# Performance work log

Measured on AMD Instinct MI355X. Metric: run time of the kernel, lower is better.

The kernel has to match this reference:

```python
import jax, jax.numpy as jnp
import numpy as np

DIM = 4096
DEPTH = 13  # complete binary tree, 2**DEPTH - 1 nodes
N_NODES = 2 ** DEPTH - 1


def setup_inputs() -> dict:
    key = jax.random.key(0)
    ks = jax.random.split(key, 9)
    inp = {
        "tree_vec": jax.random.normal(ks[0], (N_NODES, DIM), dtype=jnp.float32),
        "depth": DEPTH,
        # diagonal gate parameters (original shape (dim,1), flattened to (dim,))
        "w_for": jax.random.normal(ks[1], (DIM,), dtype=jnp.float32),
        "u_for": jax.random.normal(ks[2], (DIM,), dtype=jnp.float32),
        "b_for": jnp.zeros((DIM,), dtype=jnp.float32),
        "w_in": jax.random.normal(ks[3], (DIM,), dtype=jnp.float32),
        "u_in": jax.random.normal(ks[4], (DIM,), dtype=jnp.float32),
        "b_in": jnp.zeros((DIM,), dtype=jnp.float32),
        "w_ce": jax.random.normal(ks[5], (DIM,), dtype=jnp.float32),
        "u_ce": jax.random.normal(ks[6], (DIM,), dtype=jnp.float32),
        "b_ce": jnp.zeros((DIM,), dtype=jnp.float32),
        "w_out": jax.random.normal(ks[7], (DIM,), dtype=jnp.float32),
        "u_out": jax.random.normal(ks[8], (DIM,), dtype=jnp.float32),
        "b_out": jnp.zeros((DIM,), dtype=jnp.float32),
    }
    return inp


def _node_gates(x, h_sum, f_sum, p):
    # x, h_sum, f_sum: (n, dim); p: dict of (dim,) params
    it = jax.nn.sigmoid(p["w_in"] * x + p["u_in"] * h_sum + p["b_in"])
    gt = jnp.tanh(p["w_ce"] * x + p["u_ce"] * h_sum + p["b_ce"])
    # NOTE: faithful to the original — forget sum is added raw, not multiplied by child c
    ct = it * gt + f_sum
    ot = jax.nn.sigmoid(p["w_out"] * x + p["u_out"] * h_sum + p["b_out"])
    ht = ot * jnp.tanh(ct)
    return ht, ct


def reference(tree_vec, depth, w_for, u_for, b_for, w_in, u_in, b_in,
              w_ce, u_ce, b_ce, w_out, u_out, b_out):
    p = dict(w_for=w_for, u_for=u_for, b_for=b_for, w_in=w_in, u_in=u_in,
             b_in=b_in, w_ce=w_ce, u_ce=u_ce, b_ce=b_ce, w_out=w_out,
             u_out=u_out, b_out=b_out)
    dim = tree_vec.shape[1]

    # ---- leaf level (original gives leaves one all-zero child row) ----
    L = depth - 1
    n = 2 ** L
    x = tree_vec[2 ** L - 1: 2 ** (L + 1) - 1]          # (n, dim)
    h_sum = jnp.zeros_like(x)                            # sum of zero child h
    f_sum = jax.nn.sigmoid(w_for * x + b_for)            # u_for * 0 dropped
    h, c = _node_gates(x, h_sum, f_sum, p)

    # ---- internal levels, bottom-up ----
    for l in range(depth - 2, -1, -1):
        n = 2 ** l
        x = tree_vec[2 ** l - 1: 2 ** (l + 1) - 1]       # (n, dim)
        h_ch = h.reshape(n, 2, dim)                      # children h
        h_sum = h_ch.sum(axis=1)
        f_sum = jax.nn.sigmoid(w_for * x[:, None, :] + u_for * h_ch + b_for).sum(axis=1)
        h, c = _node_gates(x, h_sum, f_sum, p)

    # root outputs, original shape (dim, 1)
    return h[0].reshape(dim, 1), c[0].reshape(dim, 1)
```

## Files before the change

### kernel.cpp

```cpp
#include <hip/hip_runtime.h>

#define DIM 4096

typedef float v2f __attribute__((ext_vector_type(2)));

constexpr float LOG2E = 1.44269504088896340736f;
constexpr float TWO_LOG2E = 2.0f * LOG2E;

__device__ __forceinline__ float fexp2s(float x) { return __builtin_amdgcn_exp2f(x); }
__device__ __forceinline__ float frcps(float x) { return __builtin_amdgcn_rcpf(x); }

__device__ __forceinline__ v2f expv(v2f u) {
  v2f r; r.x = fexp2s(u.x); r.y = fexp2s(u.y); return r;
}
__device__ __forceinline__ v2f rcpv(v2f u) {
  v2f r; r.x = frcps(u.x); r.y = frcps(u.y); return r;
}
__device__ __forceinline__ v2f fmav(v2f a, v2f b, v2f c) {
  return __builtin_elementwise_fma(a, b, c);
}
__device__ __forceinline__ v2f eclampv(v2f u) {
  v2f c30 = {30.0f, 30.0f};
  return expv(__builtin_elementwise_min(-u, c30));
}

struct P2pk {
  v2f wf, uf, bf;
  v2f wi, ui, bi;
  v2f wc, uc, bc;
  v2f wo, uo, bo;
};

__device__ __forceinline__ v2f ldv(const float* p) { return *(const v2f*)p; }
__device__ __forceinline__ v2f ldscale(const float* p, int d2, float s) {
  return ldv(p + d2) * s;
}

__device__ __forceinline__ P2pk load_params_pk(
    int d2,
    const float* wf, const float* uf, const float* bf,
    const float* wi, const float* ui, const float* bi,
    const float* wc, const float* uc, const float* bc,
    const float* wo, const float* uo, const float* bo) {
  P2pk p;
  p.wf = ldscale(wf, d2, LOG2E);     p.uf = ldscale(uf, d2, LOG2E);     p.bf = ldscale(bf, d2, LOG2E);
  p.wi = ldscale(wi, d2, LOG2E);     p.ui = ldscale(ui, d2, LOG2E);     p.bi = ldscale(bi, d2, LOG2E);
  p.wc = ldscale(wc, d2, TWO_LOG2E); p.uc = ldscale(uc, d2, TWO_LOG2E); p.bc = ldscale(bc, d2, TWO_LOG2E);
  p.wo = ldscale(wo, d2, LOG2E);     p.uo = ldscale(uo, d2, LOG2E);     p.bo = ldscale(bo, d2, LOG2E);
  return p;
}

__device__ __forceinline__ v2f leaf_node_pk(v2f x, const P2pk& p) {
  v2f ef = eclampv(fmav(p.wf, x, p.bf));
  v2f ei = eclampv(fmav(p.wi, x, p.bi));
  v2f eg = eclampv(fmav(p.wc, x, p.bc));
  v2f sf = ef + 1.0f;
  v2f si = ei + 1.0f;
  v2f t1 = fmav(si, eg, si);
  v2f num = fmav(1.0f - eg, sf, t1);
  v2f ct = num * rcpv(t1 * sf);
  v2f eo = eclampv(fmav(p.wo, x, p.bo));
  v2f ec = expv(ct * (-TWO_LOG2E));
  v2f so = eo + 1.0f;
  return (1.0f - ec) * rcpv(fmav(so, ec, so));
}

__device__ __forceinline__ v2f inner_node_pk(v2f x, v2f hl, v2f hr, const P2pk& p) {
  v2f hs = hl + hr;
  v2f af = fmav(p.wf, x, p.bf);
  v2f e1 = eclampv(fmav(p.uf, hl, af));
  v2f e2 = eclampv(fmav(p.uf, hr, af));
  v2f s1 = e1 + 1.0f;
  v2f fD = fmav(s1, e2, s1);
  v2f fN = (e1 + e2) + 2.0f;
  v2f ei = eclampv(fmav(p.ui, hs, fmav(p.wi, x, p.bi)));
  v2f eg = eclampv(fmav(p.uc, hs, fmav(p.wc, x, p.bc)));
  v2f si = ei + 1.0f;
  v2f iD = fmav(si, eg, si);
  v2f iN = 1.0f - eg;
  v2f num = fmav(iN, fD, fN * iD);
  v2f ct = num * rcpv(fD * iD);
  v2f eo = eclampv(fmav(p.uo, hs, fmav(p.wo, x, p.bo)));
  v2f ec = expv(ct * (-TWO_LOG2E));
  v2f so = eo + 1.0f;
  return (1.0f - ec) * rcpv(fmav(so, ec, so));
}

template <int LVL>
__device__ __forceinline__ v2f subtree_h_pk(const float* __restrict__ tvd, int node,
                                            const P2pk& p) {
  if constexpr (LVL == 12) {
    v2f x = ldv(tvd + (size_t)node * DIM);
    return leaf_node_pk(x, p);
  } else {
    v2f hl = subtree_h_pk<LVL + 1>(tvd, 2 * node + 1, p);
    v2f hr = subtree_h_pk<LVL + 1>(tvd, 2 * node + 2, p);
    v2f x = ldv(tvd + (size_t)node * DIM);
    return inner_node_pk(x, hl, hr, p);
  }
}

__global__ __launch_bounds__(256, 6) void treelstm_p1(
    const float* __restrict__ tv,
    const float* __restrict__ wf, const float* __restrict__ uf, const float* __restrict__ bf,
    const float* __restrict__ wi, const float* __restrict__ ui, const float* __restrict__ bi,
    const float* __restrict__ wc, const float* __restrict__ uc, const float* __restrict__ bc,
    const float* __restrict__ wo, const float* __restrict__ uo, const float* __restrict__ bo,
    float* __restrict__ ws) {
  const int cb = blockIdx.x & 7;
  const int g  = blockIdx.x >> 3;
  const int d2 = cb * 512 + threadIdx.x * 2;
  const float* tvd = tv + d2;

  const P2pk p = load_params_pk(d2, wf, uf, bf, wi, ui, bi, wc, uc, bc, wo, uo, bo);

  const int root = 255 + g;
  v2f h = subtree_h_pk<8>(tvd, root, p);
  *(v2f*)&ws[(size_t)g * DIM + d2] = h;
}

struct Params {
  float wf, uf, bf;
  float wi, ui, bi;
  float wc, uc, bc;
  float wo, uo, bo;
};

__device__ __forceinline__ Params load_params_s(
    int d,
    const float* wf, const float* uf, const float* bf,
    const float* wi, const float* ui, const float* bi,
    const float* wc, const float* uc, const float* bc,
    const float* wo, const float* uo, const float* bo) {
  Params p;
  p.wf = wf[d] * LOG2E;     p.uf = uf[d] * LOG2E;     p.bf = bf[d] * LOG2E;
  p.wi = wi[d] * LOG2E;     p.ui = ui[d] * LOG2E;     p.bi = bi[d] * LOG2E;
  p.wc = wc[d] * TWO_LOG2E; p.uc = uc[d] * TWO_LOG2E; p.bc = bc[d] * TWO_LOG2E;
  p.wo = wo[d] * LOG2E;     p.uo = uo[d] * LOG2E;     p.bo = bo[d] * LOG2E;
  return p;
}

__device__ __forceinline__ float sig_sum2(float u1, float u2) {
  float e1 = fexp2s(-u1);
  float e2 = fexp2s(-u2);
  float s1 = 1.0f + e1;
  float den = fmaf(s1, e2, s1);
  float num = (2.0f + e1) + e2;
  return num * frcps(den);
}

__device__ __forceinline__ float sig_mul_tanh(float ui, float ug) {
  float ei = fexp2s(-ui);
  float eg = fexp2s(fminf(-ug, 60.0f));
  float si = 1.0f + ei;
  float den = fmaf(si, eg, si);
  float num = 1.0f - eg;
  return num * frcps(den);
}

__device__ __forceinline__ float inner_node_s(float x, float hl, float hr,
                                              const Params& p, float& ct_out) {
  float hs = hl + hr;
  float af = fmaf(p.wf, x, p.bf);
  float fsum = sig_sum2(fmaf(p.uf, hl, af), fmaf(p.uf, hr, af));
  float itgt = sig_mul_tanh(fmaf(p.ui, hs, fmaf(p.wi, x, p.bi)),
                            fmaf(p.uc, hs, fmaf(p.wc, x, p.bc)));
  float ct = itgt + fsum;
  ct_out = ct;
  return sig_mul_tanh(fmaf(p.uo, hs, fmaf(p.wo, x, p.bo)), ct * TWO_LOG2E);
}

template <int SPLIT, int LVL>
__device__ __forceinline__ float top_h(const float* __restrict__ tvd,
                                       const float* __restrict__ hind, int node,
                                       const Params& p, float& ct_out) {
  if constexpr (LVL == SPLIT) {
    ct_out = 0.0f;
    return hind[(size_t)(node - ((1 << SPLIT) - 1)) * DIM];
  } else {
    float cl, cr;
    float hl = top_h<SPLIT, LVL + 1>(tvd, hind, 2 * node + 1, p, cl);
    float hr = top_h<SPLIT, LVL + 1>(tvd, hind, 2 * node + 2, p, cr);
    float x = tvd[(size_t)node * DIM];
    return inner_node_s(x, hl, hr, p, ct_out);
  }
}

__global__ __launch_bounds__(256) void treelstm_ka(
    const float* __restrict__ tv,
    const float* __restrict__ wf, const float* __restrict__ uf, const float* __restrict__ bf,
    const float* __restrict__ wi, const float* __restrict__ ui, const float* __restrict__ bi,
    const float* __restrict__ wc, const float* __restrict__ uc, const float* __restrict__ bc,
    const float* __restrict__ wo, const float* __restrict__ uo, const float* __restrict__ bo,
    const float* __restrict__ A, float* __restrict__ B) {
  const int idx = blockIdx.x * 256 + threadIdx.x;
  const int d = idx & (DIM - 1);
  const int j = idx >> 12;

  const Params p = load_params_s(d, wf, uf, bf, wi, ui, bi, wc, uc, bc, wo, uo, bo);

  float ct;
  float h = top_h<8, 4>(tv + d, A + d, 15 + j, p, ct);
  B[(size_t)j * DIM + d] = h;
}

__global__ __launch_bounds__(64) void treelstm_kb(
    const float* __restrict__ tv,
    const float* __restrict__ wf, const float* __restrict__ uf, const float* __restrict__ bf,
    const float* __restrict__ wi, const float* __restrict__ ui, const float* __restrict__ bi,
    const float* __restrict__ wc, const float* __restrict__ uc, const float* __restrict__ bc,
    const float* __restrict__ wo, const float* __restrict__ uo, const float* __restrict__ bo,
    const float* __restrict__ B, float* __restrict__ out) {
  const int d = blockIdx.x * 64 + threadIdx.x;

  const Params p = load_params_s(d, wf, uf, bf, wi, ui, bi, wc, uc, bc, wo, uo, bo);

  float ct;
  float h = top_h<4, 0>(tv + d, B + d, 0, p, ct);
  out[d] = h;
  out[DIM + d] = ct;
}

extern "C" void kernel_launch(void* const* d_in, const int* in_sizes, int n_in,
                              void* d_out, int out_size, void* d_ws, size_t ws_size,
                              hipStream_t stream) {
  const float* tv = (const float*)d_in[0];
  const float* wf = (const float*)d_in[2];
  const float* uf = (const float*)d_in[3];
  const float* bf = (const float*)d_in[4];
  const float* wi = (const float*)d_in[5];
  const float* ui = (const float*)d_in[6];
  const float* bi = (const float*)d_in[7];
  const float* wc = (const float*)d_in[8];
  const float* uc = (const float*)d_in[9];
  const float* bc = (const float*)d_in[10];
  const float* wo = (const float*)d_in[11];
  const float* uo = (const float*)d_in[12];
  const float* bo = (const float*)d_in[13];

  float* out = (float*)d_out;
  float* A = (float*)d_ws;
  float* B = A + (size_t)256 * DIM;

  treelstm_p1<<<dim3(256 * 8), dim3(256), 0, stream>>>(
      tv, wf, uf, bf, wi, ui, bi, wc, uc, bc, wo, uo, bo, A);

  treelstm_ka<<<dim3(256), dim3(256), 0, stream>>>(
      tv, wf, uf, bf, wi, ui, bi, wc, uc, bc, wo, uo, bo, A, B);

  treelstm_kb<<<dim3(64), dim3(64), 0, stream>>>(
      tv, wf, uf, bf, wi, ui, bi, wc, uc, bc, wo, uo, bo, B, out);
}
```

Baseline: 42.43 us.

## Fuse top two tree-reduction kernels into one block-level kernel via shared memory

Merges the two final kernels (levels 4-7 and levels 0-3) into one kernel. Each block handles 16 dims across all 16 level-4 subtrees and then reduces levels 3..0 through shared memory with __syncthreads. This removes one kernel launch and the global round trip through buffer B. In exchange, the last levels run with most threads idle and 16-wide column accesses that are less coalesced.

```diff
diff --git a/kernel.cpp b/kernel.cpp
--- a/kernel.cpp
+++ b/kernel.cpp
@@ -186,39 +186,53 @@
   }
 }
 
-__global__ __launch_bounds__(256) void treelstm_ka(
+__global__ __launch_bounds__(256) void treelstm_top(
     const float* __restrict__ tv,
     const float* __restrict__ wf, const float* __restrict__ uf, const float* __restrict__ bf,
     const float* __restrict__ wi, const float* __restrict__ ui, const float* __restrict__ bi,
     const float* __restrict__ wc, const float* __restrict__ uc, const float* __restrict__ bc,
     const float* __restrict__ wo, const float* __restrict__ uo, const float* __restrict__ bo,
-    const float* __restrict__ A, float* __restrict__ B) {
-  const int idx = blockIdx.x * 256 + threadIdx.x;
-  const int d = idx & (DIM - 1);
-  const int j = idx >> 12;
+    const float* __restrict__ A, float* __restrict__ out) {
+  __shared__ float h4[16][17];
+  __shared__ float h3[8][17];
+  __shared__ float h2[4][17];
+  __shared__ float h1[2][17];
+
+  const int t  = threadIdx.x;
+  const int j  = t >> 4;
+  const int dl = t & 15;
+  const int d  = blockIdx.x * 16 + dl;
 
   const Params p = load_params_s(d, wf, uf, bf, wi, ui, bi, wc, uc, bc, wo, uo, bo);
 
   float ct;
-  float h = top_h<8, 4>(tv + d, A + d, 15 + j, p, ct);
-  B[(size_t)j * DIM + d] = h;
-}
-
-__global__ __launch_bounds__(64) void treelstm_kb(
-    const float* __restrict__ tv,
-    const float* __restrict__ wf, const float* __restrict__ uf, const float* __restrict__ bf,
-    const float* __restrict__ wi, const float* __restrict__ ui, const float* __restrict__ bi,
-    const float* __restrict__ wc, const float* __restrict__ uc, const float* __restrict__ bc,
-    const float* __restrict__ wo, const float* __restrict__ uo, const float* __restrict__ bo,
-    const float* __restrict__ B, float* __restrict__ out) {
-  const int d = blockIdx.x * 64 + threadIdx.x;
-
-  const Params p = load_params_s(d, wf, uf, bf, wi, ui, bi, wc, uc, bc, wo, uo, bo);
-
-  float ct;
-  float h = top_h<4, 0>(tv + d, B + d, 0, p, ct);
-  out[d] = h;
-  out[DIM + d] = ct;
+  h4[j][dl] = top_h<8, 4>(tv + d, A + d, 15 + j, p, ct);
+  __syncthreads();
+
+  if (j < 8) {
+    float x = tv[(size_t)(7 + j) * DIM + d];
+    h3[j][dl] = inner_node_s(x, h4[2 * j][dl], h4[2 * j + 1][dl], p, ct);
+  }
+  __syncthreads();
+
+  if (j < 4) {
+    float x = tv[(size_t)(3 + j) * DIM + d];
+    h2[j][dl] = inner_node_s(x, h3[2 * j][dl], h3[2 * j + 1][dl], p, ct);
+  }
+  __syncthreads();
+
+  if (j < 2) {
+    float x = tv[(size_t)(1 + j) * DIM + d];
+    h1[j][dl] = inner_node_s(x, h2[2 * j][dl], h2[2 * j + 1][dl], p, ct);
+  }
+  __syncthreads();
+
+  if (j == 0) {
+    float x = tv[d];
+    float h = inner_node_s(x, h1[0][dl], h1[1][dl], p, ct);
+    out[d] = h;
+    out[DIM + d] = ct;
+  }
 }
 
 extern "C" void kernel_launch(void* const* d_in, const int* in_sizes, int n_in,
@@ -240,14 +254,10 @@
 
   float* out = (float*)d_out;
   float* A = (float*)d_ws;
-  float* B = A + (size_t)256 * DIM;
 
   treelstm_p1<<<dim3(256 * 8), dim3(256), 0, stream>>>(
       tv, wf, uf, bf, wi, ui, bi, wc, uc, bc, wo, uo, bo, A);
 
-  treelstm_ka<<<dim3(256), dim3(256), 0, stream>>>(
-      tv, wf, uf, bf, wi, ui, bi, wc, uc, bc, wo, uo, bo, A, B);
-
-  treelstm_kb<<<dim3(64), dim3(64), 0, stream>>>(
-      tv, wf, uf, bf, wi, ui, bi, wc, uc, bc, wo, uo, bo, B, out);
-}
+  treelstm_top<<<dim3(256), dim3(256), 0, stream>>>(
+      tv, wf, uf, bf, wi, ui, bi, wc, uc, bc, wo, uo, bo, A, out);
+}
```

Measured after the change: 40.81 us (median of 2 runs). 3.8% less time.
